# Performance work log

Measured on AMD Instinct MI355X. Metric: run time of the kernel, lower is better.

Reference implementation:

```python
import jax, jax.numpy as jnp
import numpy as np

N = 100000      # nodes
E = 2000000     # edges
F_NODE = 32     # num_node_features
F_EDGE = 16     # num_edge_features
HID = 128       # size_conv_layers
G = 4096        # num graphs (molecules)
NCLS = 2        # class_weights.shape[0]
NEG = 0.01      # LeakyReLU default negative slope
BN_EPS = 1e-5


def _bn(h, gamma, beta):
    # torch BatchNorm1d training-mode forward: biased batch stats over node dim
    m = jnp.mean(h, axis=0)
    v = jnp.var(h, axis=0)
    return (h - m) * jax.lax.rsqrt(v + BN_EPS) * gamma + beta


def _lrelu(h):
    return jnp.where(h > 0, h, NEG * h)


def setup_inputs() -> dict:
    key = jax.random.key(0)
    ks = jax.random.split(key, 64)
    d = {}
    d["x"] = jax.random.normal(ks[0], (N, F_NODE), dtype=jnp.float32)
    d["edge_index"] = jax.random.randint(ks[1], (2, E), 0, N, dtype=jnp.int64)
    d["edge_attr"] = jax.random.normal(ks[2], (E, F_EDGE), dtype=jnp.float32)
    d["batch"] = jnp.sort(jax.random.randint(ks[3], (N,), 0, G, dtype=jnp.int64))
    dims = [F_NODE, HID, HID]  # in_channels of each conv layer
    i = 4
    for l, ic in enumerate(dims):
        d[f"eps{l}"] = jnp.zeros((), jnp.float32)                                # GINE train_eps init 0
        d[f"ew{l}"] = 0.05 * jax.random.normal(ks[i], (F_EDGE, ic), jnp.float32); i += 1
        d[f"eb{l}"] = jnp.zeros((ic,), jnp.float32)
        d[f"w1{l}"] = 0.05 * jax.random.normal(ks[i], (ic, HID), jnp.float32); i += 1
        d[f"b1{l}"] = jnp.zeros((HID,), jnp.float32)
        d[f"g1{l}"] = jnp.ones((HID,), jnp.float32)
        d[f"be1{l}"] = jnp.zeros((HID,), jnp.float32)
        d[f"w2{l}"] = 0.05 * jax.random.normal(ks[i], (HID, HID), jnp.float32); i += 1
        d[f"b2{l}"] = jnp.zeros((HID,), jnp.float32)
        d[f"g2{l}"] = jnp.ones((HID,), jnp.float32)
        d[f"be2{l}"] = jnp.zeros((HID,), jnp.float32)
    d["wf"] = 0.05 * jax.random.normal(ks[i], (2 * HID, NCLS), jnp.float32)
    d["bf"] = jnp.zeros((NCLS,), jnp.float32)
    return d


def _forward(x, edge_index, edge_attr, batch, layers, wf, bf):
    src = edge_index[0]  # x_j (messages flow source->target in PyG)
    dst = edge_index[1]  # x_i
    for (eps, ew, eb, w1, b1, g1, be1, w2, b2, g2, be2) in layers:
        e = edge_attr @ ew + eb                     # [E, in_ch]
        msg = jax.nn.relu(x[src] + e)               # GINE message
        agg = jax.ops.segment_sum(msg, dst, num_segments=N)
        h = (1.0 + eps) * x + agg                   # [N, in_ch]
        h = _lrelu(_bn(h @ w1 + b1, g1, be1))       # nn: Lin->BN->LeakyReLU
        h = h @ w2 + b2                             # nn: Lin
        x = _lrelu(_bn(h, g2, be2))                 # outer BN + LeakyReLU
    pool = jax.ops.segment_sum(x, batch, num_segments=G)  # global_add_pool
    x_cat = jnp.concatenate([x, pool[batch]], axis=1)      # repeat_interleave broadcast
    logits = x_cat @ wf + bf
    return jax.nn.softmax(logits, axis=1)


def reference(x, edge_index, edge_attr, batch,
              eps0, ew0, eb0, w10, b10, g10, be10, w20, b20, g20, be20,
              eps1, ew1, eb1, w11, b11, g11, be11, w21, b21, g21, be21,
              eps2, ew2, eb2, w12, b12, g12, be12, w22, b22, g22, be22,
              wf, bf):
    layers = [
        (eps0, ew0, eb0, w10, b10, g10, be10, w20, b20, g20, be20),
        (eps1, ew1, eb1, w11, b11, g11, be11, w21, b21, g21, be21),
        (eps2, ew2, eb2, w12, b12, g12, be12, w22, b22, g22, be22),
    ]
    return _forward(x, edge_index, edge_attr, batch, layers, wf, bf)
```

## Files before the change

### kernel.cpp

```cpp
#include <hip/hip_runtime.h>

#define GEMM_GRID 512
#define GNUM 4096

typedef __attribute__((ext_vector_type(8))) short short8_t;
typedef __attribute__((ext_vector_type(4))) float f32x4;

__device__ __forceinline__ float bf2f(unsigned short u) {
    union { unsigned int i; float f; } v; v.i = ((unsigned int)u) << 16; return v.f;
}
__device__ __forceinline__ unsigned short f2bf(float f) {
    union { float f; unsigned int i; } v; v.f = f;
    unsigned int b = v.i + 0x7FFFu + ((v.i >> 16) & 1u);
    return (unsigned short)(b >> 16);
}

__global__ __launch_bounds__(256) void hist_kernel(
    const int* __restrict__ dstv, int* __restrict__ cnt, int E)
{
    int i = blockIdx.x * 256 + threadIdx.x;
    if (i < E) atomicAdd(&cnt[dstv[i] + 1], 1);
}

__global__ __launch_bounds__(256) void scan_block_kernel(
    int* __restrict__ data, int* __restrict__ bsum, int n)
{
    __shared__ int s[256];
    int tid = threadIdx.x;
    int base = blockIdx.x * 1024 + tid * 4;
    int v[4]; int run = 0;
    #pragma unroll
    for (int i = 0; i < 4; i++) {
        int x = (base + i < n) ? data[base + i] : 0;
        run += x; v[i] = run;
    }
    s[tid] = run; __syncthreads();
    for (int off = 1; off < 256; off <<= 1) {
        int t = (tid >= off) ? s[tid - off] : 0;
        __syncthreads();
        s[tid] += t;
        __syncthreads();
    }
    int excl = s[tid] - run;
    #pragma unroll
    for (int i = 0; i < 4; i++)
        if (base + i < n) data[base + i] = v[i] + excl;
    if (tid == 255) bsum[blockIdx.x] = s[255];
}

__global__ __launch_bounds__(128) void scan_carry_kernel(int* __restrict__ bsum, int nb)
{
    __shared__ int s[128];
    int tid = threadIdx.x;
    int orig = (tid < nb) ? bsum[tid] : 0;
    s[tid] = orig; __syncthreads();
    for (int off = 1; off < 128; off <<= 1) {
        int t = (tid >= off) ? s[tid - off] : 0;
        __syncthreads();
        s[tid] += t;
        __syncthreads();
    }
    if (tid < nb) bsum[tid] = s[tid] - orig;
}

__global__ __launch_bounds__(256) void scan_add_kernel(
    int* __restrict__ data, const int* __restrict__ bsum,
    int* __restrict__ cursor, int n, int N)
{
    int i = blockIdx.x * 256 + threadIdx.x;
    if (i < n) {
        int v = data[i] + bsum[i >> 10];
        data[i] = v;
        if (i < N) cursor[i] = v;
    }
}

__global__ __launch_bounds__(256) void scatter_kernel(
    const int* __restrict__ dstv, int* __restrict__ cursor,
    int* __restrict__ perm, int E)
{
    int i = blockIdx.x * 256 + threadIdx.x;
    if (i < E) {
        int p = atomicAdd(&cursor[dstv[i]], 1);
        perm[p] = i;
    }
}

__global__ __launch_bounds__(256) void reorder_kernel(
    const float* __restrict__ ea, const int* __restrict__ srcv,
    const int* __restrict__ perm, float* __restrict__ eap,
    int* __restrict__ srcp, int E)
{
    int i = blockIdx.x * 256 + threadIdx.x;
    int p = i >> 2, q = i & 3;
    if (p >= E) return;
    int e = perm[p];
    float4 v = reinterpret_cast<const float4*>(ea)[e * 4 + q];
    reinterpret_cast<float4*>(eap)[p * 4 + q] = v;
    if (q == 0) srcp[p] = srcv[e];
}

template<bool RO>
__global__ __launch_bounds__(256) void gather_kernel128(
    const float* __restrict__ ea, const int* __restrict__ srcv,
    const int* __restrict__ perm, const int* __restrict__ off,
    const float* __restrict__ ew, const float* __restrict__ ebias,
    const float* __restrict__ epsp, const float* __restrict__ x,
    float* __restrict__ agg, int N)
{
    int lane = threadIdx.x & 63;
    int n = __builtin_amdgcn_readfirstlane((int)((blockIdx.x * 256 + threadIdx.x) >> 6));
    if (n >= N) return;
    const int c0 = lane * 2;
    float ew0[16], ew1[16];
    #pragma unroll
    for (int k = 0; k < 16; k++) {
        float2 w = *reinterpret_cast<const float2*>(&ew[k * 128 + c0]);
        ew0[k] = w.x; ew1[k] = w.y;
    }
    const float eb0 = ebias[c0], eb1 = ebias[c0 + 1];
    float acc0 = 0.f, acc1 = 0.f;
    int p = off[n];
    const int end = off[n + 1];
    for (; p + 2 <= end; p += 2) {
        int e0 = RO ? p : perm[p];
        int e1 = RO ? (p + 1) : perm[p + 1];
        int s0 = srcv[e0], s1 = srcv[e1];
        const float4* ap0 = reinterpret_cast<const float4*>(ea + (size_t)e0 * 16);
        const float4* ap1 = reinterpret_cast<const float4*>(ea + (size_t)e1 * 16);
        float av[16], bv[16];
        #pragma unroll
        for (int q = 0; q < 4; q++) {
            float4 t = ap0[q]; av[4*q]=t.x; av[4*q+1]=t.y; av[4*q+2]=t.z; av[4*q+3]=t.w;
            float4 u = ap1[q]; bv[4*q]=u.x; bv[4*q+1]=u.y; bv[4*q+2]=u.z; bv[4*q+3]=u.w;
        }
        float2 xv0 = *reinterpret_cast<const float2*>(&x[(size_t)s0 * 128 + c0]);
        float2 xv1 = *reinterpret_cast<const float2*>(&x[(size_t)s1 * 128 + c0]);
        float u0 = eb0, u1 = eb1, w0 = eb0, w1 = eb1;
        #pragma unroll
        for (int k = 0; k < 16; k++) {
            u0 = fmaf(av[k], ew0[k], u0);
            u1 = fmaf(av[k], ew1[k], u1);
            w0 = fmaf(bv[k], ew0[k], w0);
            w1 = fmaf(bv[k], ew1[k], w1);
        }
        acc0 += fmaxf(xv0.x + u0, 0.f) + fmaxf(xv1.x + w0, 0.f);
        acc1 += fmaxf(xv0.y + u1, 0.f) + fmaxf(xv1.y + w1, 0.f);
    }
    if (p < end) {
        int e0 = RO ? p : perm[p];
        int s0 = srcv[e0];
        const float4* ap0 = reinterpret_cast<const float4*>(ea + (size_t)e0 * 16);
        float av[16];
        #pragma unroll
        for (int q = 0; q < 4; q++) {
            float4 t = ap0[q]; av[4*q]=t.x; av[4*q+1]=t.y; av[4*q+2]=t.z; av[4*q+3]=t.w;
        }
        float2 xv0 = *reinterpret_cast<const float2*>(&x[(size_t)s0 * 128 + c0]);
        float u0 = eb0, u1 = eb1;
        #pragma unroll
        for (int k = 0; k < 16; k++) {
            u0 = fmaf(av[k], ew0[k], u0);
            u1 = fmaf(av[k], ew1[k], u1);
        }
        acc0 += fmaxf(xv0.x + u0, 0.f);
        acc1 += fmaxf(xv0.y + u1, 0.f);
    }
    float2 xn = *reinterpret_cast<const float2*>(&x[(size_t)n * 128 + c0]);
    float s = 1.f + epsp[0];
    float2 o;
    o.x = fmaf(xn.x, s, acc0);
    o.y = fmaf(xn.y, s, acc1);
    *reinterpret_cast<float2*>(&agg[(size_t)n * 128 + c0]) = o;
}

template<bool RO>
__global__ __launch_bounds__(256) void gather_kernel32(
    const float* __restrict__ ea, const int* __restrict__ srcv,
    const int* __restrict__ perm, const int* __restrict__ off,
    const float* __restrict__ ew, const float* __restrict__ ebias,
    const float* __restrict__ epsp, const float* __restrict__ x,
    float* __restrict__ agg, int N)
{
    int lane = threadIdx.x & 63;
    int n = __builtin_amdgcn_readfirstlane((int)((blockIdx.x * 256 + threadIdx.x) >> 6));
    if (n >= N) return;
    const int h = lane >> 5;
    const int c = lane & 31;
    float ewr[16];
    #pragma unroll
    for (int k = 0; k < 16; k++) ewr[k] = ew[k * 32 + c];
    const float ebr = ebias[c];
    float acc = 0.f;
    const int p0 = off[n], end = off[n + 1];
    for (int p = p0; p < end; p += 8) {
        int i0 = p + h, i1 = p + 2 + h, i2 = p + 4 + h, i3 = p + 6 + h;
        bool v0 = i0 < end, v1 = i1 < end, v2 = i2 < end, v3 = i3 < end;
        int j0 = v0 ? i0 : p, j1 = v1 ? i1 : p, j2 = v2 ? i2 : p, j3 = v3 ? i3 : p;
        int e0 = RO ? j0 : perm[j0];
        int e1 = RO ? j1 : perm[j1];
        int e2 = RO ? j2 : perm[j2];
        int e3 = RO ? j3 : perm[j3];
        int s0 = srcv[e0], s1 = srcv[e1], s2 = srcv[e2], s3 = srcv[e3];
        const float4* a0p = reinterpret_cast<const float4*>(ea + (size_t)e0 * 16);
        const float4* a1p = reinterpret_cast<const float4*>(ea + (size_t)e1 * 16);
        const float4* a2p = reinterpret_cast<const float4*>(ea + (size_t)e2 * 16);
        const float4* a3p = reinterpret_cast<const float4*>(ea + (size_t)e3 * 16);
        float a0v[16], a1v[16], a2v[16], a3v[16];
        #pragma unroll
        for (int q = 0; q < 4; q++) {
            float4 t0 = a0p[q]; a0v[4*q]=t0.x; a0v[4*q+1]=t0.y; a0v[4*q+2]=t0.z; a0v[4*q+3]=t0.w;
            float4 t1 = a1p[q]; a1v[4*q]=t1.x; a1v[4*q+1]=t1.y; a1v[4*q+2]=t1.z; a1v[4*q+3]=t1.w;
            float4 t2 = a2p[q]; a2v[4*q]=t2.x; a2v[4*q+1]=t2.y; a2v[4*q+2]=t2.z; a2v[4*q+3]=t2.w;
            float4 t3 = a3p[q]; a3v[4*q]=t3.x; a3v[4*q+1]=t3.y; a3v[4*q+2]=t3.z; a3v[4*q+3]=t3.w;
        }
        float x0v = x[(size_t)s0 * 32 + c];
        float x1v = x[(size_t)s1 * 32 + c];
        float x2v = x[(size_t)s2 * 32 + c];
        float x3v = x[(size_t)s3 * 32 + c];
        float u0 = ebr, u1 = ebr, u2 = ebr, u3 = ebr;
        #pragma unroll
        for (int k = 0; k < 16; k++) {
            u0 = fmaf(a0v[k], ewr[k], u0);
            u1 = fmaf(a1v[k], ewr[k], u1);
            u2 = fmaf(a2v[k], ewr[k], u2);
            u3 = fmaf(a3v[k], ewr[k], u3);
        }
        acc += v0 ? fmaxf(x0v + u0, 0.f) : 0.f;
        acc += v1 ? fmaxf(x1v + u1, 0.f) : 0.f;
        acc += v2 ? fmaxf(x2v + u2, 0.f) : 0.f;
        acc += v3 ? fmaxf(x3v + u3, 0.f) : 0.f;
    }
    acc += __shfl_xor(acc, 32);
    if (lane < 32) {
        float s = 1.f + epsp[0];
        agg[(size_t)n * 32 + c] = fmaf(x[(size_t)n * 32 + c], s, acc);
    }
}

template<int K, bool BN_IN>
__global__ __launch_bounds__(256, 3) void gemm_mfma_kernel(
    const float* __restrict__ A, const float* __restrict__ ss,
    const float* __restrict__ W, const float* __restrict__ bias,
    float* __restrict__ out, float* __restrict__ stats, int N, int ntiles)
{
    constexpr int PA = K + 8;
    __shared__ unsigned short As_hi[32 * PA];
    __shared__ unsigned short As_lo[32 * PA];
    __shared__ unsigned short Wt[128 * PA];
    __shared__ float scale_s[K];
    __shared__ float shift_s[K];
    const int tid = threadIdx.x;
    const int w = tid >> 6;
    const int lane = tid & 63;
    const int quad = lane >> 4;
    const int l16 = lane & 15;
    const int rbase = (w & 1) * 16;
    const int nbase = (w >> 1) * 4;

    for (int idx = tid; idx < K * 128; idx += 256) {
        int k = idx >> 7, nn = idx & 127;
        Wt[nn * PA + k] = f2bf(W[idx]);
    }
    if (BN_IN) {
        for (int i = tid; i < K; i += 256) { scale_s[i] = ss[i]; shift_s[i] = ss[K + i]; }
    }
    float bcol[4];
    #pragma unroll
    for (int nt = 0; nt < 4; nt++) bcol[nt] = bias[(nbase + nt) * 16 + l16];
    float csum[4] = {0.f, 0.f, 0.f, 0.f}, csq[4] = {0.f, 0.f, 0.f, 0.f};

    constexpr int C8 = K / 8;

    for (int tile = blockIdx.x; tile < ntiles; tile += gridDim.x) {
        const int row0 = tile * 32;
        __syncthreads();
        for (int cid = tid; cid < 32 * C8; cid += 256) {
            int row = cid / C8, c8 = cid % C8;
            int r = row0 + row;
            float f[8];
            if (r < N) {
                float4 u0 = *reinterpret_cast<const float4*>(&A[(size_t)r * K + c8 * 8]);
                float4 u1 = *reinterpret_cast<const float4*>(&A[(size_t)r * K + c8 * 8 + 4]);
                f[0]=u0.x; f[1]=u0.y; f[2]=u0.z; f[3]=u0.w;
                f[4]=u1.x; f[5]=u1.y; f[6]=u1.z; f[7]=u1.w;
            } else {
                #pragma unroll
                for (int j = 0; j < 8; j++) f[j] = 0.f;
            }
            if (BN_IN) {
                int kb = c8 * 8;
                #pragma unroll
                for (int j = 0; j < 8; j++) {
                    float v = fmaf(f[j], scale_s[kb + j], shift_s[kb + j]);
                    f[j] = (v > 0.f) ? v : 0.01f * v;
                }
            }
            unsigned int hi[4], lo[4];
            #pragma unroll
            for (int j = 0; j < 4; j++) {
                unsigned short h0 = f2bf(f[2*j]);
                unsigned short h1 = f2bf(f[2*j + 1]);
                unsigned short l0 = f2bf(f[2*j]     - bf2f(h0));
                unsigned short l1 = f2bf(f[2*j + 1] - bf2f(h1));
                hi[j] = (unsigned int)h0 | ((unsigned int)h1 << 16);
                lo[j] = (unsigned int)l0 | ((unsigned int)l1 << 16);
            }
            *reinterpret_cast<uint4*>(&As_hi[row * PA + c8 * 8]) = make_uint4(hi[0], hi[1], hi[2], hi[3]);
            *reinterpret_cast<uint4*>(&As_lo[row * PA + c8 * 8]) = make_uint4(lo[0], lo[1], lo[2], lo[3]);
        }
        __syncthreads();

        f32x4 acc[4];
        #pragma unroll
        for (int nt = 0; nt < 4; nt++) { f32x4 z = {0.f,0.f,0.f,0.f}; acc[nt] = z; }
        #pragma unroll
        for (int chunk = 0; chunk < K / 32; chunk++) {
            short8_t ahi = *reinterpret_cast<const short8_t*>(
                &As_hi[(rbase + l16) * PA + chunk * 32 + quad * 8]);
            short8_t alo = *reinterpret_cast<const short8_t*>(
                &As_lo[(rbase + l16) * PA + chunk * 32 + quad * 8]);
            #pragma unroll
            for (int nt = 0; nt < 4; nt++) {
                short8_t bfr = *reinterpret_cast<const short8_t*>(
                    &Wt[((nbase + nt) * 16 + l16) * PA + chunk * 32 + quad * 8]);
                acc[nt] = __builtin_amdgcn_mfma_f32_16x16x32_bf16(alo, bfr, acc[nt], 0, 0, 0);
                acc[nt] = __builtin_amdgcn_mfma_f32_16x16x32_bf16(ahi, bfr, acc[nt], 0, 0, 0);
            }
        }
        const int rb = row0 + rbase + quad * 4;
        #pragma unroll
        for (int nt = 0; nt < 4; nt++) {
            #pragma unroll
            for (int rg = 0; rg < 4; rg++) {
                int r = rb + rg;
                if (r < N) {
                    float v = acc[nt][rg] + bcol[nt];
                    out[(size_t)r * 128 + (nbase + nt) * 16 + l16] = v;
                    csum[nt] += v; csq[nt] += v * v;
                }
            }
        }
    }
    #pragma unroll
    for (int nt = 0; nt < 4; nt++) {
        float s = csum[nt]; s += __shfl_xor(s, 16); s += __shfl_xor(s, 32);
        float q = csq[nt];  q += __shfl_xor(q, 16); q += __shfl_xor(q, 32);
        if (quad == 0) {
            int col = (nbase + nt) * 16 + l16;
            atomicAdd(&stats[col], s);
            atomicAdd(&stats[128 + col], q);
        }
    }
}

__global__ __launch_bounds__(128) void transform_stats(
    const float* __restrict__ stats, float invN,
    const float* __restrict__ g, const float* __restrict__ be,
    float* __restrict__ ssout)
{
    int c = threadIdx.x;
    float mean = stats[c] * invN;
    float var = fmaxf(stats[128 + c] * invN - mean * mean, 0.f);
    float inv = rsqrtf(var + 1e-5f);
    float sc = g[c] * inv;
    ssout[c] = sc;
    ssout[128 + c] = be[c] - mean * sc;
}

__global__ __launch_bounds__(256) void bn_lrelu_kernel(
    const float* __restrict__ U, const float* __restrict__ ss,
    float* __restrict__ xo, int total4)
{
    int i = blockIdx.x * 256 + threadIdx.x;
    if (i >= total4) return;
    int cq = (i & 31) * 4;
    float4 v = reinterpret_cast<const float4*>(U)[i];
    float s0 = ss[cq], s1 = ss[cq + 1], s2 = ss[cq + 2], s3 = ss[cq + 3];
    float h0 = ss[128 + cq], h1 = ss[129 + cq], h2 = ss[130 + cq], h3 = ss[131 + cq];
    v.x = fmaf(v.x, s0, h0); v.x = (v.x > 0.f) ? v.x : 0.01f * v.x;
    v.y = fmaf(v.y, s1, h1); v.y = (v.y > 0.f) ? v.y : 0.01f * v.y;
    v.z = fmaf(v.z, s2, h2); v.z = (v.z > 0.f) ? v.z : 0.01f * v.z;
    v.w = fmaf(v.w, s3, h3); v.w = (v.w > 0.f) ? v.w : 0.01f * v.w;
    reinterpret_cast<float4*>(xo)[i] = v;
}

__global__ __launch_bounds__(256) void pool_kernel(
    const float* __restrict__ x3, const int* __restrict__ batch,
    float* __restrict__ pool, int N)
{
    int w = (blockIdx.x * 256 + threadIdx.x) >> 6;
    int lane = threadIdx.x & 63;
    int n0 = w * 32;
    if (n0 >= N) return;
    int n1 = min(n0 + 32, N);
    int c0 = lane * 2;
    float a0 = 0.f, a1 = 0.f;
    int cur = batch[n0];
    for (int n = n0; n < n1; ++n) {
        int b = batch[n];
        if (b != cur) {
            atomicAdd(&pool[(size_t)cur * 128 + c0], a0);
            atomicAdd(&pool[(size_t)cur * 128 + c0 + 1], a1);
            a0 = a1 = 0.f; cur = b;
        }
        float2 v = *reinterpret_cast<const float2*>(&x3[(size_t)n * 128 + c0]);
        a0 += v.x; a1 += v.y;
    }
    atomicAdd(&pool[(size_t)cur * 128 + c0], a0);
    atomicAdd(&pool[(size_t)cur * 128 + c0 + 1], a1);
}

__global__ __launch_bounds__(256) void final_kernel(
    const float* __restrict__ x3, const float* __restrict__ pool,
    const int* __restrict__ batch, const float* __restrict__ wf,
    const float* __restrict__ bf, float* __restrict__ out, int N)
{
    __shared__ float wf_s[512];
    int tid = threadIdx.x;
    for (int i = tid; i < 512; i += 256) wf_s[i] = wf[i];
    __syncthreads();
    int wid = tid >> 6, lane = tid & 63;
    int n = blockIdx.x * 4 + wid;
    if (n >= N) return;
    int b = batch[n];
    float v0 = x3[(size_t)n * 128 + lane];
    float v1 = x3[(size_t)n * 128 + 64 + lane];
    float p0 = pool[(size_t)b * 128 + lane];
    float p1 = pool[(size_t)b * 128 + 64 + lane];
    float a0 = v0 * wf_s[lane * 2]       + v1 * wf_s[(64 + lane) * 2]
             + p0 * wf_s[(128 + lane) * 2] + p1 * wf_s[(192 + lane) * 2];
    float a1 = v0 * wf_s[lane * 2 + 1]       + v1 * wf_s[(64 + lane) * 2 + 1]
             + p0 * wf_s[(128 + lane) * 2 + 1] + p1 * wf_s[(192 + lane) * 2 + 1];
    #pragma unroll
    for (int off = 32; off >= 1; off >>= 1) {
        a0 += __shfl_down(a0, off);
        a1 += __shfl_down(a1, off);
    }
    if (lane == 0) {
        a0 += bf[0]; a1 += bf[1];
        float mx = fmaxf(a0, a1);
        float e0 = __expf(a0 - mx), e1 = __expf(a1 - mx);
        float inv = 1.f / (e0 + e1);
        out[(size_t)n * 2]     = e0 * inv;
        out[(size_t)n * 2 + 1] = e1 * inv;
    }
}

extern "C" void kernel_launch(void* const* d_in, const int* in_sizes, int n_in,
                              void* d_out, int out_size, void* d_ws, size_t ws_size,
                              hipStream_t stream)
{
    const float* x0    = (const float*)d_in[0];
    const int*   ei    = (const int*)d_in[1];
    const float* ea    = (const float*)d_in[2];
    const int*   batch = (const int*)d_in[3];
    const int E = in_sizes[1] / 2;
    const int N = in_sizes[3];
    const int* srcv = ei;
    const int* dstv = ei + E;
    const float* wf = (const float*)d_in[37];
    const float* bfp = (const float*)d_in[38];
    float* out = (float*)d_out;
    const float invN = 1.0f / (float)N;
    const int ntiles = (N + 31) / 32;

    const size_t base_f = (size_t)2 * N * 128 + (size_t)GNUM * 128 + 12 * 256
                        + (size_t)(N + 1) + (size_t)N + 128 + (size_t)E;
    const size_t full_f = base_f + (size_t)E * 16 + (size_t)E;
    const bool ro = (ws_size >= full_f * 4);

    float* ws = (float*)d_ws;
    size_t o = 0;
    float* xA    = ws + o; o += (size_t)N * 128;
    float* xB    = ws + o; o += (size_t)N * 128;
    float* eap   = ws + o; o += ro ? (size_t)E * 16 : 0;
    float* poolb = ws + o; o += (size_t)GNUM * 128;
    float* statsb= ws + o; o += 6 * 256;
    float* ssb   = ws + o; o += 6 * 256;
    int* srcp    = (int*)(ws + o); o += ro ? (size_t)E : 0;
    int* off     = (int*)(ws + o); o += (size_t)(N + 1);
    int* cursor  = (int*)(ws + o); o += (size_t)N;
    int* bsumb   = (int*)(ws + o); o += 128;
    int* perm    = (int*)(ws + o);

    hipMemsetAsync(off, 0, (size_t)(N + 1) * sizeof(int), stream);
    hipMemsetAsync(statsb, 0, (size_t)6 * 256 * sizeof(float), stream);
    hipMemsetAsync(poolb, 0, (size_t)GNUM * 128 * sizeof(float), stream);
    hist_kernel<<<(E + 255) / 256, 256, 0, stream>>>(dstv, off, E);
    const int n1 = N + 1;
    const int nb = (n1 + 1023) / 1024;
    scan_block_kernel<<<nb, 256, 0, stream>>>(off, bsumb, n1);
    scan_carry_kernel<<<1, 128, 0, stream>>>(bsumb, nb);
    scan_add_kernel<<<(n1 + 255) / 256, 256, 0, stream>>>(off, bsumb, cursor, n1, N);
    scatter_kernel<<<(E + 255) / 256, 256, 0, stream>>>(dstv, cursor, perm, E);
    if (ro)
        reorder_kernel<<<(E * 4 + 255) / 256, 256, 0, stream>>>(ea, srcv, perm, eap, srcp, E);

    const float* g_ea  = ro ? eap  : ea;
    const int*   g_src = ro ? srcp : srcv;
    const int gather_blocks = (N + 3) / 4;

    for (int l = 0; l < 3; l++) {
        const int C = (l == 0) ? 32 : 128;
        int bidx = 4 + l * 11;
        const float* epsp = (const float*)d_in[bidx + 0];
        const float* ew   = (const float*)d_in[bidx + 1];
        const float* eb   = (const float*)d_in[bidx + 2];
        const float* w1   = (const float*)d_in[bidx + 3];
        const float* b1   = (const float*)d_in[bidx + 4];
        const float* g1   = (const float*)d_in[bidx + 5];
        const float* be1  = (const float*)d_in[bidx + 6];
        const float* w2   = (const float*)d_in[bidx + 7];
        const float* b2   = (const float*)d_in[bidx + 8];
        const float* g2   = (const float*)d_in[bidx + 9];
        const float* be2  = (const float*)d_in[bidx + 10];
        float* st1 = statsb + (size_t)(l * 2) * 256;
        float* st2 = statsb + (size_t)(l * 2 + 1) * 256;
        float* ss1 = ssb + (size_t)(l * 2) * 256;
        float* ss2 = ssb + (size_t)(l * 2 + 1) * 256;

        if (C == 32) {
            if (ro) gather_kernel32<true><<<gather_blocks, 256, 0, stream>>>(
                        g_ea, g_src, perm, off, ew, eb, epsp, x0, xB, N);
            else    gather_kernel32<false><<<gather_blocks, 256, 0, stream>>>(
                        g_ea, g_src, perm, off, ew, eb, epsp, x0, xB, N);
            gemm_mfma_kernel<32, false><<<GEMM_GRID, 256, 0, stream>>>(
                xB, nullptr, w1, b1, xA, st1, N, ntiles);
        } else {
            if (ro) gather_kernel128<true><<<gather_blocks, 256, 0, stream>>>(
                        g_ea, g_src, perm, off, ew, eb, epsp, xB, xA, N);
            else    gather_kernel128<false><<<gather_blocks, 256, 0, stream>>>(
                        g_ea, g_src, perm, off, ew, eb, epsp, xB, xA, N);
            gemm_mfma_kernel<128, false><<<GEMM_GRID, 256, 0, stream>>>(
                xA, nullptr, w1, b1, xA, st1, N, ntiles);
        }
        transform_stats<<<1, 128, 0, stream>>>(st1, invN, g1, be1, ss1);
        gemm_mfma_kernel<128, true><<<GEMM_GRID, 256, 0, stream>>>(
            xA, ss1, w2, b2, xA, st2, N, ntiles);
        transform_stats<<<1, 128, 0, stream>>>(st2, invN, g2, be2, ss2);
        int t4 = N * 32;
        bn_lrelu_kernel<<<(t4 + 255) / 256, 256, 0, stream>>>(xA, ss2, xB, t4);
    }
    pool_kernel<<<((N + 31) / 32 * 64 + 255) / 256, 256, 0, stream>>>(xB, batch, poolb, N);
    final_kernel<<<(N + 3) / 4, 256, 0, stream>>>(xB, poolb, batch, wf, bfp, out, N);
}
```

Baseline: 1.514 ms.

## Fold outer BN+LeakyReLU into consumer kernels and drop stats transform launches

Removes the standalone bn_lrelu pass and both transform_stats launches per layer. The next layer's gather, the pool and the final kernel now apply the BN scale/shift and LeakyReLU on the fly to raw GEMM output, computing scale/shift from the raw stats, and the GEMM does the same for its BN input. This saves a full N×128 read+write pass per layer and several tiny launches. In exchange the gather does extra per-edge math and buffers ping-pong. The layer-0 gather is also narrowed from 8 to 4 edges per iteration, and the bf16 hi/lo split is rewritten with byte perms and truncation instead of rounding.

Measured after the change: 1.487 ms. Within noise of the previous version (-1.8%).

```diff
diff --git a/kernel.cpp b/kernel.cpp
--- a/kernel.cpp
+++ b/kernel.cpp
@@ -14,6 +14,7 @@
     unsigned int b = v.i + 0x7FFFu + ((v.i >> 16) & 1u);
     return (unsigned short)(b >> 16);
 }
+__device__ __forceinline__ float lrelu(float v) { return v > 0.f ? v : 0.01f * v; }
 
 __global__ __launch_bounds__(256) void hist_kernel(
     const int* __restrict__ dstv, int* __restrict__ cnt, int E)
@@ -101,7 +102,7 @@
 }
 
 template<bool RO>
-__global__ __launch_bounds__(256) void gather_kernel128(
+__global__ __launch_bounds__(256) void gather_kernel32(
     const float* __restrict__ ea, const int* __restrict__ srcv,
     const int* __restrict__ perm, const int* __restrict__ off,
     const float* __restrict__ ew, const float* __restrict__ ebias,
@@ -111,7 +112,73 @@
     int lane = threadIdx.x & 63;
     int n = __builtin_amdgcn_readfirstlane((int)((blockIdx.x * 256 + threadIdx.x) >> 6));
     if (n >= N) return;
+    const int h = lane >> 5;
+    const int c = lane & 31;
+    float ewr[16];
+    #pragma unroll
+    for (int k = 0; k < 16; k++) ewr[k] = ew[k * 32 + c];
+    const float ebr = ebias[c];
+    float acc = 0.f;
+    const int p0 = off[n], end = off[n + 1];
+    for (int p = p0; p < end; p += 4) {
+        int pa = p + h, pb = p + 2 + h;
+        bool va = pa < end, vb = pb < end;
+        int ia = va ? pa : p;
+        int ib = vb ? pb : p;
+        int eA = RO ? ia : perm[ia];
+        int eB = RO ? ib : perm[ib];
+        int sa = srcv[eA], sb = srcv[eB];
+        const float4* apA = reinterpret_cast<const float4*>(ea + (size_t)eA * 16);
+        const float4* apB = reinterpret_cast<const float4*>(ea + (size_t)eB * 16);
+        float av[16], bv[16];
+        #pragma unroll
+        for (int q = 0; q < 4; q++) {
+            float4 t = apA[q]; av[4*q]=t.x; av[4*q+1]=t.y; av[4*q+2]=t.z; av[4*q+3]=t.w;
+            float4 u = apB[q]; bv[4*q]=u.x; bv[4*q+1]=u.y; bv[4*q+2]=u.z; bv[4*q+3]=u.w;
+        }
+        float xa = x[(size_t)sa * 32 + c];
+        float xb = x[(size_t)sb * 32 + c];
+        float ua = ebr, ub = ebr;
+        #pragma unroll
+        for (int k = 0; k < 16; k++) {
+            ua = fmaf(av[k], ewr[k], ua);
+            ub = fmaf(bv[k], ewr[k], ub);
+        }
+        acc += va ? fmaxf(xa + ua, 0.f) : 0.f;
+        acc += vb ? fmaxf(xb + ub, 0.f) : 0.f;
+    }
+    acc += __shfl_xor(acc, 32);
+    if (lane < 32) {
+        float s = 1.f + epsp[0];
+        agg[(size_t)n * 32 + c] = fmaf(x[(size_t)n * 32 + c], s, acc);
+    }
+}
+
+template<bool RO>
+__global__ __launch_bounds__(256) void gather_kernel128_bn(
+    const float* __restrict__ ea, const int* __restrict__ srcv,
+    const int* __restrict__ perm, const int* __restrict__ off,
+    const float* __restrict__ ew, const float* __restrict__ ebias,
+    const float* __restrict__ epsp, const float* __restrict__ U,
+    const float* __restrict__ stats, const float* __restrict__ g,
+    const float* __restrict__ be, float invN,
+    float* __restrict__ agg, int N)
+{
+    int lane = threadIdx.x & 63;
+    int n = __builtin_amdgcn_readfirstlane((int)((blockIdx.x * 256 + threadIdx.x) >> 6));
+    if (n >= N) return;
     const int c0 = lane * 2;
+    float sc0, sh0, sc1, sh1;
+    {
+        float m0 = stats[c0] * invN;
+        float v0 = fmaxf(stats[128 + c0] * invN - m0 * m0, 0.f);
+        sc0 = g[c0] * rsqrtf(v0 + 1e-5f);
+        sh0 = be[c0] - m0 * sc0;
+        float m1 = stats[c0 + 1] * invN;
+        float v1 = fmaxf(stats[128 + c0 + 1] * invN - m1 * m1, 0.f);
+        sc1 = g[c0 + 1] * rsqrtf(v1 + 1e-5f);
+        sh1 = be[c0 + 1] - m1 * sc1;
+    }
     float ew0[16], ew1[16];
     #pragma unroll
     for (int k = 0; k < 16; k++) {
@@ -134,8 +201,12 @@
             float4 t = ap0[q]; av[4*q]=t.x; av[4*q+1]=t.y; av[4*q+2]=t.z; av[4*q+3]=t.w;
             float4 u = ap1[q]; bv[4*q]=u.x; bv[4*q+1]=u.y; bv[4*q+2]=u.z; bv[4*q+3]=u.w;
         }
-        float2 xv0 = *reinterpret_cast<const float2*>(&x[(size_t)s0 * 128 + c0]);
-        float2 xv1 = *reinterpret_cast<const float2*>(&x[(size_t)s1 * 128 + c0]);
+        float2 xv0 = *reinterpret_cast<const float2*>(&U[(size_t)s0 * 128 + c0]);
+        float2 xv1 = *reinterpret_cast<const float2*>(&U[(size_t)s1 * 128 + c0]);
+        float x00 = lrelu(fmaf(xv0.x, sc0, sh0));
+        float x01 = lrelu(fmaf(xv0.y, sc1, sh1));
+        float x10 = lrelu(fmaf(xv1.x, sc0, sh0));
+        float x11 = lrelu(fmaf(xv1.y, sc1, sh1));
         float u0 = eb0, u1 = eb1, w0 = eb0, w1 = eb1;
         #pragma unroll
         for (int k = 0; k < 16; k++) {
@@ -144,8 +215,8 @@
             w0 = fmaf(bv[k], ew0[k], w0);
             w1 = fmaf(bv[k], ew1[k], w1);
         }
-        acc0 += fmaxf(xv0.x + u0, 0.f) + fmaxf(xv1.x + w0, 0.f);
-        acc1 += fmaxf(xv0.y + u1, 0.f) + fmaxf(xv1.y + w1, 0.f);
+        acc0 += fmaxf(x00 + u0, 0.f) + fmaxf(x10 + w0, 0.f);
+        acc1 += fmaxf(x01 + u1, 0.f) + fmaxf(x11 + w1, 0.f);
     }
     if (p < end) {
         int e0 = RO ? p : perm[p];
@@ -156,93 +227,35 @@
         for (int q = 0; q < 4; q++) {
             float4 t = ap0[q]; av[4*q]=t.x; av[4*q+1]=t.y; av[4*q+2]=t.z; av[4*q+3]=t.w;
         }
-        float2 xv0 = *reinterpret_cast<const float2*>(&x[(size_t)s0 * 128 + c0]);
+        float2 xv0 = *reinterpret_cast<const float2*>(&U[(size_t)s0 * 128 + c0]);
+        float x00 = lrelu(fmaf(xv0.x, sc0, sh0));
+        float x01 = lrelu(fmaf(xv0.y, sc1, sh1));
         float u0 = eb0, u1 = eb1;
         #pragma unroll
         for (int k = 0; k < 16; k++) {
             u0 = fmaf(av[k], ew0[k], u0);
             u1 = fmaf(av[k], ew1[k], u1);
         }
-        acc0 += fmaxf(xv0.x + u0, 0.f);
-        acc1 += fmaxf(xv0.y + u1, 0.f);
-    }
-    float2 xn = *reinterpret_cast<const float2*>(&x[(size_t)n * 128 + c0]);
+        acc0 += fmaxf(x00 + u0, 0.f);
+        acc1 += fmaxf(x01 + u1, 0.f);
+    }
+    float2 xn = *reinterpret_cast<const float2*>(&U[(size_t)n * 128 + c0]);
+    float xn0 = lrelu(fmaf(xn.x, sc0, sh0));
+    float xn1 = lrelu(fmaf(xn.y, sc1, sh1));
     float s = 1.f + epsp[0];
     float2 o;
-    o.x = fmaf(xn.x, s, acc0);
-    o.y = fmaf(xn.y, s, acc1);
+    o.x = fmaf(xn0, s, acc0);
+    o.y = fmaf(xn1, s, acc1);
     *reinterpret_cast<float2*>(&agg[(size_t)n * 128 + c0]) = o;
-}
-
-template<bool RO>
-__global__ __launch_bounds__(256) void gather_kernel32(
-    const float* __restrict__ ea, const int* __restrict__ srcv,
-    const int* __restrict__ perm, const int* __restrict__ off,
-    const float* __restrict__ ew, const float* __restrict__ ebias,
-    const float* __restrict__ epsp, const float* __restrict__ x,
-    float* __restrict__ agg, int N)
-{
-    int lane = threadIdx.x & 63;
-    int n = __builtin_amdgcn_readfirstlane((int)((blockIdx.x * 256 + threadIdx.x) >> 6));
-    if (n >= N) return;
-    const int h = lane >> 5;
-    const int c = lane & 31;
-    float ewr[16];
-    #pragma unroll
-    for (int k = 0; k < 16; k++) ewr[k] = ew[k * 32 + c];
-    const float ebr = ebias[c];
-    float acc = 0.f;
-    const int p0 = off[n], end = off[n + 1];
-    for (int p = p0; p < end; p += 8) {
-        int i0 = p + h, i1 = p + 2 + h, i2 = p + 4 + h, i3 = p + 6 + h;
-        bool v0 = i0 < end, v1 = i1 < end, v2 = i2 < end, v3 = i3 < end;
-        int j0 = v0 ? i0 : p, j1 = v1 ? i1 : p, j2 = v2 ? i2 : p, j3 = v3 ? i3 : p;
-        int e0 = RO ? j0 : perm[j0];
-        int e1 = RO ? j1 : perm[j1];
-        int e2 = RO ? j2 : perm[j2];
-        int e3 = RO ? j3 : perm[j3];
-        int s0 = srcv[e0], s1 = srcv[e1], s2 = srcv[e2], s3 = srcv[e3];
-        const float4* a0p = reinterpret_cast<const float4*>(ea + (size_t)e0 * 16);
-        const float4* a1p = reinterpret_cast<const float4*>(ea + (size_t)e1 * 16);
-        const float4* a2p = reinterpret_cast<const float4*>(ea + (size_t)e2 * 16);
-        const float4* a3p = reinterpret_cast<const float4*>(ea + (size_t)e3 * 16);
-        float a0v[16], a1v[16], a2v[16], a3v[16];
-        #pragma unroll
-        for (int q = 0; q < 4; q++) {
-            float4 t0 = a0p[q]; a0v[4*q]=t0.x; a0v[4*q+1]=t0.y; a0v[4*q+2]=t0.z; a0v[4*q+3]=t0.w;
-            float4 t1 = a1p[q]; a1v[4*q]=t1.x; a1v[4*q+1]=t1.y; a1v[4*q+2]=t1.z; a1v[4*q+3]=t1.w;
-            float4 t2 = a2p[q]; a2v[4*q]=t2.x; a2v[4*q+1]=t2.y; a2v[4*q+2]=t2.z; a2v[4*q+3]=t2.w;
-            float4 t3 = a3p[q]; a3v[4*q]=t3.x; a3v[4*q+1]=t3.y; a3v[4*q+2]=t3.z; a3v[4*q+3]=t3.w;
-        }
-        float x0v = x[(size_t)s0 * 32 + c];
-        float x1v = x[(size_t)s1 * 32 + c];
-        float x2v = x[(size_t)s2 * 32 + c];
-        float x3v = x[(size_t)s3 * 32 + c];
-        float u0 = ebr, u1 = ebr, u2 = ebr, u3 = ebr;
-        #pragma unroll
-        for (int k = 0; k < 16; k++) {
-            u0 = fmaf(a0v[k], ewr[k], u0);
-            u1 = fmaf(a1v[k], ewr[k], u1);
-            u2 = fmaf(a2v[k], ewr[k], u2);
-            u3 = fmaf(a3v[k], ewr[k], u3);
-        }
-        acc += v0 ? fmaxf(x0v + u0, 0.f) : 0.f;
-        acc += v1 ? fmaxf(x1v + u1, 0.f) : 0.f;
-        acc += v2 ? fmaxf(x2v + u2, 0.f) : 0.f;
-        acc += v3 ? fmaxf(x3v + u3, 0.f) : 0.f;
-    }
-    acc += __shfl_xor(acc, 32);
-    if (lane < 32) {
-        float s = 1.f + epsp[0];
-        agg[(size_t)n * 32 + c] = fmaf(x[(size_t)n * 32 + c], s, acc);
-    }
 }
 
 template<int K, bool BN_IN>
 __global__ __launch_bounds__(256, 3) void gemm_mfma_kernel(
-    const float* __restrict__ A, const float* __restrict__ ss,
+    const float* __restrict__ A,
+    const float* __restrict__ stats_in, const float* __restrict__ g,
+    const float* __restrict__ be, float invN,
     const float* __restrict__ W, const float* __restrict__ bias,
-    float* __restrict__ out, float* __restrict__ stats, int N, int ntiles)
+    float* __restrict__ out, float* __restrict__ stats_out, int N, int ntiles)
 {
     constexpr int PA = K + 8;
     __shared__ unsigned short As_hi[32 * PA];
@@ -263,7 +276,13 @@
         Wt[nn * PA + k] = f2bf(W[idx]);
     }
     if (BN_IN) {
-        for (int i = tid; i < K; i += 256) { scale_s[i] = ss[i]; shift_s[i] = ss[K + i]; }
+        for (int i = tid; i < K; i += 256) {
+            float m = stats_in[i] * invN;
+            float va = fmaxf(stats_in[K + i] * invN - m * m, 0.f);
+            float sc = g[i] * rsqrtf(va + 1e-5f);
+            scale_s[i] = sc;
+            shift_s[i] = be[i] - m * sc;
+        }
     }
     float bcol[4];
     #pragma unroll
@@ -291,20 +310,18 @@
             if (BN_IN) {
                 int kb = c8 * 8;
                 #pragma unroll
-                for (int j = 0; j < 8; j++) {
-                    float v = fmaf(f[j], scale_s[kb + j], shift_s[kb + j]);
-                    f[j] = (v > 0.f) ? v : 0.01f * v;
-                }
+                for (int j = 0; j < 8; j++)
+                    f[j] = lrelu(fmaf(f[j], scale_s[kb + j], shift_s[kb + j]));
             }
             unsigned int hi[4], lo[4];
             #pragma unroll
             for (int j = 0; j < 4; j++) {
-                unsigned short h0 = f2bf(f[2*j]);
-                unsigned short h1 = f2bf(f[2*j + 1]);
-                unsigned short l0 = f2bf(f[2*j]     - bf2f(h0));
-                unsigned short l1 = f2bf(f[2*j + 1] - bf2f(h1));
-                hi[j] = (unsigned int)h0 | ((unsigned int)h1 << 16);
-                lo[j] = (unsigned int)l0 | ((unsigned int)l1 << 16);
+                unsigned int b0 = __float_as_uint(f[2*j]);
+                unsigned int b1 = __float_as_uint(f[2*j + 1]);
+                hi[j] = __builtin_amdgcn_perm(b1, b0, 0x07060302u);
+                float l0 = f[2*j]     - __uint_as_float(b0 & 0xffff0000u);
+                float l1 = f[2*j + 1] - __uint_as_float(b1 & 0xffff0000u);
+                lo[j] = __builtin_amdgcn_perm(__float_as_uint(l1), __float_as_uint(l0), 0x07060302u);
             }
             *reinterpret_cast<uint4*>(&As_hi[row * PA + c8 * 8]) = make_uint4(hi[0], hi[1], hi[2], hi[3]);
             *reinterpret_cast<uint4*>(&As_lo[row * PA + c8 * 8]) = make_uint4(lo[0], lo[1], lo[2], lo[3]);
@@ -348,45 +365,16 @@
         float q = csq[nt];  q += __shfl_xor(q, 16); q += __shfl_xor(q, 32);
         if (quad == 0) {
             int col = (nbase + nt) * 16 + l16;
-            atomicAdd(&stats[col], s);
-            atomicAdd(&stats[128 + col], q);
-        }
-    }
-}
-
-__global__ __launch_bounds__(128) void transform_stats(
-    const float* __restrict__ stats, float invN,
-    const float* __restrict__ g, const float* __restrict__ be,
-    float* __restrict__ ssout)
-{
-    int c = threadIdx.x;
-    float mean = stats[c] * invN;
-    float var = fmaxf(stats[128 + c] * invN - mean * mean, 0.f);
-    float inv = rsqrtf(var + 1e-5f);
-    float sc = g[c] * inv;
-    ssout[c] = sc;
-    ssout[128 + c] = be[c] - mean * sc;
-}
-
-__global__ __launch_bounds__(256) void bn_lrelu_kernel(
-    const float* __restrict__ U, const float* __restrict__ ss,
-    float* __restrict__ xo, int total4)
-{
-    int i = blockIdx.x * 256 + threadIdx.x;
-    if (i >= total4) return;
-    int cq = (i & 31) * 4;
-    float4 v = reinterpret_cast<const float4*>(U)[i];
-    float s0 = ss[cq], s1 = ss[cq + 1], s2 = ss[cq + 2], s3 = ss[cq + 3];
-    float h0 = ss[128 + cq], h1 = ss[129 + cq], h2 = ss[130 + cq], h3 = ss[131 + cq];
-    v.x = fmaf(v.x, s0, h0); v.x = (v.x > 0.f) ? v.x : 0.01f * v.x;
-    v.y = fmaf(v.y, s1, h1); v.y = (v.y > 0.f) ? v.y : 0.01f * v.y;
-    v.z = fmaf(v.z, s2, h2); v.z = (v.z > 0.f) ? v.z : 0.01f * v.z;
-    v.w = fmaf(v.w, s3, h3); v.w = (v.w > 0.f) ? v.w : 0.01f * v.w;
-    reinterpret_cast<float4*>(xo)[i] = v;
-}
-
-__global__ __launch_bounds__(256) void pool_kernel(
-    const float* __restrict__ x3, const int* __restrict__ batch,
+            atomicAdd(&stats_out[col], s);
+            atomicAdd(&stats_out[128 + col], q);
+        }
+    }
+}
+
+__global__ __launch_bounds__(256) void pool_kernel_bn(
+    const float* __restrict__ U, const int* __restrict__ batch,
+    const float* __restrict__ stats, const float* __restrict__ g,
+    const float* __restrict__ be, float invN,
     float* __restrict__ pool, int N)
 {
     int w = (blockIdx.x * 256 + threadIdx.x) >> 6;
@@ -395,6 +383,17 @@
     if (n0 >= N) return;
     int n1 = min(n0 + 32, N);
     int c0 = lane * 2;
+    float sc0, sh0, sc1, sh1;
+    {
+        float m0 = stats[c0] * invN;
+        float v0 = fmaxf(stats[128 + c0] * invN - m0 * m0, 0.f);
+        sc0 = g[c0] * rsqrtf(v0 + 1e-5f);
+        sh0 = be[c0] - m0 * sc0;
+        float m1 = stats[c0 + 1] * invN;
+        float v1 = fmaxf(stats[128 + c0 + 1] * invN - m1 * m1, 0.f);
+        sc1 = g[c0 + 1] * rsqrtf(v1 + 1e-5f);
+        sh1 = be[c0 + 1] - m1 * sc1;
+    }
     float a0 = 0.f, a1 = 0.f;
     int cur = batch[n0];
     for (int n = n0; n < n1; ++n) {
@@ -404,17 +403,21 @@
             atomicAdd(&pool[(size_t)cur * 128 + c0 + 1], a1);
             a0 = a1 = 0.f; cur = b;
         }
-        float2 v = *reinterpret_cast<const float2*>(&x3[(size_t)n * 128 + c0]);
-        a0 += v.x; a1 += v.y;
+        float2 v = *reinterpret_cast<const float2*>(&U[(size_t)n * 128 + c0]);
+        a0 += lrelu(fmaf(v.x, sc0, sh0));
+        a1 += lrelu(fmaf(v.y, sc1, sh1));
     }
     atomicAdd(&pool[(size_t)cur * 128 + c0], a0);
     atomicAdd(&pool[(size_t)cur * 128 + c0 + 1], a1);
 }
 
-__global__ __launch_bounds__(256) void final_kernel(
-    const float* __restrict__ x3, const float* __restrict__ pool,
-    const int* __restrict__ batch, const float* __restrict__ wf,
-    const float* __restrict__ bf, float* __restrict__ out, int N)
+__global__ __launch_bounds__(256) void final_kernel_bn(
+    const float* __restrict__ U, const float* __restrict__ pool,
+    const int* __restrict__ batch,
+    const float* __restrict__ stats, const float* __restrict__ g,
+    const float* __restrict__ be, float invN,
+    const float* __restrict__ wf, const float* __restrict__ bf,
+    float* __restrict__ out, int N)
 {
     __shared__ float wf_s[512];
     int tid = threadIdx.x;
@@ -423,11 +426,23 @@
     int wid = tid >> 6, lane = tid & 63;
     int n = blockIdx.x * 4 + wid;
     if (n >= N) return;
+    int cA = lane, cB = 64 + lane;
+    float scA, shA, scB, shB;
+    {
+        float mA = stats[cA] * invN;
+        float vA = fmaxf(stats[128 + cA] * invN - mA * mA, 0.f);
+        scA = g[cA] * rsqrtf(vA + 1e-5f);
+        shA = be[cA] - mA * scA;
+        float mB = stats[cB] * invN;
+        float vB = fmaxf(stats[128 + cB] * invN - mB * mB, 0.f);
+        scB = g[cB] * rsqrtf(vB + 1e-5f);
+        shB = be[cB] - mB * scB;
+    }
     int b = batch[n];
-    float v0 = x3[(size_t)n * 128 + lane];
-    float v1 = x3[(size_t)n * 128 + 64 + lane];
-    float p0 = pool[(size_t)b * 128 + lane];
-    float p1 = pool[(size_t)b * 128 + 64 + lane];
+    float v0 = lrelu(fmaf(U[(size_t)n * 128 + cA], scA, shA));
+    float v1 = lrelu(fmaf(U[(size_t)n * 128 + cB], scB, shB));
+    float p0 = pool[(size_t)b * 128 + cA];
+    float p1 = pool[(size_t)b * 128 + cB];
     float a0 = v0 * wf_s[lane * 2]       + v1 * wf_s[(64 + lane) * 2]
              + p0 * wf_s[(128 + lane) * 2] + p1 * wf_s[(192 + lane) * 2];
     float a1 = v0 * wf_s[lane * 2 + 1]       + v1 * wf_s[(64 + lane) * 2 + 1]
@@ -465,7 +480,7 @@
     const float invN = 1.0f / (float)N;
     const int ntiles = (N + 31) / 32;
 
-    const size_t base_f = (size_t)2 * N * 128 + (size_t)GNUM * 128 + 12 * 256
+    const size_t base_f = (size_t)2 * N * 128 + (size_t)GNUM * 128 + 6 * 256
                         + (size_t)(N + 1) + (size_t)N + 128 + (size_t)E;
     const size_t full_f = base_f + (size_t)E * 16 + (size_t)E;
     const bool ro = (ws_size >= full_f * 4);
@@ -477,7 +492,6 @@
     float* eap   = ws + o; o += ro ? (size_t)E * 16 : 0;
     float* poolb = ws + o; o += (size_t)GNUM * 128;
     float* statsb= ws + o; o += 6 * 256;
-    float* ssb   = ws + o; o += 6 * 256;
     int* srcp    = (int*)(ws + o); o += ro ? (size_t)E : 0;
     int* off     = (int*)(ws + o); o += (size_t)(N + 1);
     int* cursor  = (int*)(ws + o); o += (size_t)N;
@@ -500,6 +514,10 @@
     const float* g_ea  = ro ? eap  : ea;
     const int*   g_src = ro ? srcp : srcv;
     const int gather_blocks = (N + 3) / 4;
+
+    float* Uprev = nullptr;
+    const float *pg = nullptr, *pbe = nullptr;
+    float* pstats = nullptr;
 
     for (int l = 0; l < 3; l++) {
         const int C = (l == 0) ? 32 : 128;
@@ -517,31 +535,35 @@
         const float* be2  = (const float*)d_in[bidx + 10];
         float* st1 = statsb + (size_t)(l * 2) * 256;
         float* st2 = statsb + (size_t)(l * 2 + 1) * 256;
-        float* ss1 = ssb + (size_t)(l * 2) * 256;
-        float* ss2 = ssb + (size_t)(l * 2 + 1) * 256;
-
-        if (C == 32) {
+
+        if (l == 0) {
             if (ro) gather_kernel32<true><<<gather_blocks, 256, 0, stream>>>(
                         g_ea, g_src, perm, off, ew, eb, epsp, x0, xB, N);
             else    gather_kernel32<false><<<gather_blocks, 256, 0, stream>>>(
                         g_ea, g_src, perm, off, ew, eb, epsp, x0, xB, N);
             gemm_mfma_kernel<32, false><<<GEMM_GRID, 256, 0, stream>>>(
-                xB, nullptr, w1, b1, xA, st1, N, ntiles);
+                xB, nullptr, nullptr, nullptr, invN, w1, b1, xA, st1, N, ntiles);
+            gemm_mfma_kernel<128, true><<<GEMM_GRID, 256, 0, stream>>>(
+                xA, st1, g1, be1, invN, w2, b2, xA, st2, N, ntiles);
+            Uprev = xA;
         } else {
-            if (ro) gather_kernel128<true><<<gather_blocks, 256, 0, stream>>>(
-                        g_ea, g_src, perm, off, ew, eb, epsp, xB, xA, N);
-            else    gather_kernel128<false><<<gather_blocks, 256, 0, stream>>>(
-                        g_ea, g_src, perm, off, ew, eb, epsp, xB, xA, N);
+            float* dst = (Uprev == xA) ? xB : xA;
+            if (ro) gather_kernel128_bn<true><<<gather_blocks, 256, 0, stream>>>(
+                        g_ea, g_src, perm, off, ew, eb, epsp, Uprev,
+                        pstats, pg, pbe, invN, dst, N);
+            else    gather_kernel128_bn<false><<<gather_blocks, 256, 0, stream>>>(
+                        g_ea, g_src, perm, off, ew, eb, epsp, Uprev,
+                        pstats, pg, pbe, invN, dst, N);
             gemm_mfma_kernel<128, false><<<GEMM_GRID, 256, 0, stream>>>(
-                xA, nullptr, w1, b1, xA, st1, N, ntiles);
-        }
-        transform_stats<<<1, 128, 0, stream>>>(st1, invN, g1, be1, ss1);
-        gemm_mfma_kernel<128, true><<<GEMM_GRID, 256, 0, stream>>>(
-            xA, ss1, w2, b2, xA, st2, N, ntiles);
-        transform_stats<<<1, 128, 0, stream>>>(st2, invN, g2, be2, ss2);
-        int t4 = N * 32;
-        bn_lrelu_kernel<<<(t4 + 255) / 256, 256, 0, stream>>>(xA, ss2, xB, t4);
-    }
-    pool_kernel<<<((N + 31) / 32 * 64 + 255) / 256, 256, 0, stream>>>(xB, batch, poolb, N);
-    final_kernel<<<(N + 3) / 4, 256, 0, stream>>>(xB, poolb, batch, wf, bfp, out, N);
-}
+                dst, nullptr, nullptr, nullptr, invN, w1, b1, dst, st1, N, ntiles);
+            gemm_mfma_kernel<128, true><<<GEMM_GRID, 256, 0, stream>>>(
+                dst, st1, g1, be1, invN, w2, b2, dst, st2, N, ntiles);
+            Uprev = dst;
+        }
+        pstats = st2; pg = g2; pbe = be2;
+    }
+    pool_kernel_bn<<<((N + 31) / 32 * 64 + 255) / 256, 256, 0, stream>>>(
+        Uprev, batch, pstats, pg, pbe, invN, poolb, N);
+    final_kernel_bn<<<(N + 3) / 4, 256, 0, stream>>>(
+        Uprev, poolb, batch, pstats, pg, pbe, invN, wf, bfp, out, N);
+}
```
